# Kernel tuning notes

Hardware: AMD Instinct MI355X
Metric: run time of the kernel (lower is better)

Reference implementation:

```python
import jax, jax.numpy as jnp
import numpy as np

VOCAB = 256
HDC_DIM = 4096
DECAY = 0.95
B, T = 8, 2048


def setup_inputs() -> dict:
    key = jax.random.key(0)
    k_cb, k_idx = jax.random.split(key)
    # bipolar codebook: sign of gaussian, zeros mapped to +1 (prob-0 event but faithful)
    cb = jnp.sign(jax.random.normal(k_cb, (VOCAB, HDC_DIM), dtype=jnp.float32))
    cb = jnp.where(cb == 0, 1.0, cb)
    idx = jax.random.randint(k_idx, (B, T), 0, VOCAB)
    return {"char_codebook": cb, "idx": idx}


def _encode_trigrams(char_codebook, idx):
    chars = char_codebook[idx]                       # (B, T, D)
    chars_m1 = jnp.roll(chars, 1, axis=1).at[:, 0, :].set(0.0)
    chars_m2 = jnp.roll(chars, 2, axis=1).at[:, :2, :].set(0.0)
    trigrams = chars * jnp.roll(chars_m1, 1, axis=-1) * jnp.roll(chars_m2, 2, axis=-1)
    return 0.7 * trigrams + 0.3 * chars


def _decay_matrix(T, dtype):
    i = jnp.arange(T)
    diffs = (i[:, None] - i[None, :]).astype(dtype)  # (T, T)
    m = jnp.where(diffs >= 0, jnp.asarray(DECAY, dtype) ** diffs, 0.0)
    return m / jnp.sum(m, axis=-1, keepdims=True)    # row-normalized causal decay


def reference(char_codebook, idx):
    hdc = _encode_trigrams(char_codebook, idx)       # (B, T, D)
    M = _decay_matrix(hdc.shape[1], hdc.dtype)       # (T, T)
    # context[t] = sum_i M[t, i] * hdc[i]  -> one dense matmul as in the original
    return jnp.einsum("ts,bsd->btd", M, hdc)
```

## Files before the change

### kernel.cpp

```cpp
#include <hip/hip_runtime.h>


#define VOCAB   256
#define D_      4096
#define T_      2048
#define B_      8
#define DEC     0.95f
#define CHUNK   32
#define NCH     (T_/CHUNK)
#define THREADS 128
#define DGRP    (D_/(THREADS*8))
#define ROWB    (D_/8)

__device__ unsigned char g_P1[VOCAB*ROWB];
__device__ unsigned char g_P2[VOCAB*ROWB];
__device__ unsigned char g_P3[VOCAB*ROWB];
__device__ float g_invn[T_];
__device__ float g_S[B_*NCH*D_];
__device__ float g_C[B_*NCH*D_];

__global__ __launch_bounds__(256) void pack_kernel(const float* __restrict__ cb) {
    int gid = blockIdx.x * 256 + threadIdx.x;
    int r   = gid >> 9;
    int byt = gid & 511;
    const float* row = cb + r * D_;
    unsigned b1 = 0, b2 = 0, b3 = 0;
#pragma unroll
    for (int j = 0; j < 8; ++j) {
        int d = byt * 8 + j;
        unsigned s1 = __float_as_uint(row[d]) >> 31;
        unsigned s2 = __float_as_uint(row[(d - 1) & (D_ - 1)]) >> 31;
        unsigned s3 = __float_as_uint(row[(d - 2) & (D_ - 1)]) >> 31;
        b1 |= s1 << j; b2 |= s2 << j; b3 |= s3 << j;
    }
    g_P1[gid] = (unsigned char)b1;
    g_P2[gid] = (unsigned char)b2;
    g_P3[gid] = (unsigned char)b3;
    if (gid < T_)
        g_invn[gid] = (1.0f - DEC) / (1.0f - powf(DEC, (float)(gid + 1)));
}

__device__ __forceinline__ void bind_step(unsigned ub1, unsigned n8,
                                          float magp, float magn, float* acc) {
#pragma unroll
    for (int j = 0; j < 8; ++j) {
        float mag    = ((n8 >> j) & 1u) ? magn : magp;
        unsigned sgn = (ub1 << (31 - j)) & 0x80000000u;
        float v      = __uint_as_float(__float_as_uint(mag) ^ sgn);
        acc[j] = fmaf(acc[j], DEC, v);
    }
}

__global__ __launch_bounds__(THREADS) void states_kernel(const int* __restrict__ idx) {
    const int b  = blockIdx.z;
    const int ch = blockIdx.y;
    const int dg = blockIdx.x;
    const int t0 = ch * CHUNK;
    const int lo = (t0 - 2 > 0) ? (t0 - 2) : 0;

    __shared__ int sidx[CHUNK + 2];
    if (threadIdx.x < (unsigned)(t0 + CHUNK - lo))
        sidx[threadIdx.x] = idx[b * T_ + lo + threadIdx.x];
    __syncthreads();

    const int i = dg * THREADS + threadIdx.x;
    float acc[8];
#pragma unroll
    for (int j = 0; j < 8; ++j) acc[j] = 0.0f;

#pragma unroll 4
    for (int k = 0; k < CHUNK; ++k) {
        int t = t0 + k;
        int r1 = sidx[t - lo];
        unsigned ub1 = g_P1[r1 * ROWB + i];
        unsigned n8 = 0; float magp = 1.0f, magn = -0.4f;
        if (t >= 2) {
            int r2 = sidx[t - 1 - lo], r3 = sidx[t - 2 - lo];
            n8 = (unsigned)(g_P2[r2 * ROWB + i] ^ g_P3[r3 * ROWB + i]);
        } else { magp = 0.3f; magn = 0.3f; }
        bind_step(ub1, n8, magp, magn, acc);
    }

    float* S = g_S + (size_t)(b * NCH + ch) * D_ + (size_t)i * 8;
    ((float4*)S)[0] = make_float4(acc[0], acc[1], acc[2], acc[3]);
    ((float4*)S)[1] = make_float4(acc[4], acc[5], acc[6], acc[7]);
}

__global__ __launch_bounds__(256) void carry_kernel() {
    int g = blockIdx.x * 256 + threadIdx.x;
    int b = g >> 12;
    int d = g & (D_ - 1);
    float dch = powf(DEC, (float)CHUNK);
    float c = 0.0f;
#pragma unroll 8
    for (int ch = 0; ch < NCH; ++ch) {
        size_t o = (size_t)(b * NCH + ch) * D_ + d;
        g_C[o] = c;
        c = fmaf(c, dch, g_S[o]);
    }
}

__global__ __launch_bounds__(THREADS) void emit_kernel(const int* __restrict__ idx,
                                                       float* __restrict__ out) {
    const int b  = blockIdx.z;
    const int ch = blockIdx.y;
    const int dg = blockIdx.x;
    const int t0 = ch * CHUNK;
    const int lo = (t0 - 2 > 0) ? (t0 - 2) : 0;

    __shared__ int   sidx[CHUNK + 2];
    __shared__ float sinv[CHUNK];
    if (threadIdx.x < (unsigned)(t0 + CHUNK - lo))
        sidx[threadIdx.x] = idx[b * T_ + lo + threadIdx.x];
    if (threadIdx.x < CHUNK)
        sinv[threadIdx.x] = g_invn[t0 + threadIdx.x];
    __syncthreads();

    const int i = dg * THREADS + threadIdx.x;

    const float* C = g_C + (size_t)(b * NCH + ch) * D_ + (size_t)i * 8;
    float4 c0 = ((const float4*)C)[0];
    float4 c1 = ((const float4*)C)[1];
    float acc[8] = {c0.x, c0.y, c0.z, c0.w, c1.x, c1.y, c1.z, c1.w};

    float* ob = out + (size_t)(b * T_) * D_ + (size_t)i * 8;
#pragma unroll 4
    for (int k = 0; k < CHUNK; ++k) {
        int t = t0 + k;
        int r1 = sidx[t - lo];
        unsigned ub1 = g_P1[r1 * ROWB + i];
        unsigned n8 = 0; float magp = 1.0f, magn = -0.4f;
        if (t >= 2) {
            int r2 = sidx[t - 1 - lo], r3 = sidx[t - 2 - lo];
            n8 = (unsigned)(g_P2[r2 * ROWB + i] ^ g_P3[r3 * ROWB + i]);
        } else { magp = 0.3f; magn = 0.3f; }
        bind_step(ub1, n8, magp, magn, acc);

        float invn = sinv[k];
        float4* o = (float4*)(ob + (size_t)t * D_);
        o[0] = make_float4(acc[0]*invn, acc[1]*invn, acc[2]*invn, acc[3]*invn);
        o[1] = make_float4(acc[4]*invn, acc[5]*invn, acc[6]*invn, acc[7]*invn);
    }
}

extern "C" void kernel_launch(void* const* d_in, const int* in_sizes, int n_in,
                              void* d_out, int out_size, void* d_ws, size_t ws_size,
                              hipStream_t stream) {
    const float* cb  = (const float*)d_in[0];
    const int*   idx = (const int*)d_in[1];
    float*       out = (float*)d_out;

    pack_kernel  <<<dim3((VOCAB * ROWB) / 256), dim3(256), 0, stream>>>(cb);
    states_kernel<<<dim3(DGRP, NCH, B_), dim3(THREADS), 0, stream>>>(idx);
    carry_kernel <<<dim3((B_ * D_) / 256), dim3(256), 0, stream>>>();
    emit_kernel  <<<dim3(DGRP, NCH, B_), dim3(THREADS), 0, stream>>>(idx, out);
}
```

Before: 304.1 us.

## Replace chunked scan with warm-up recurrence fused into single emit kernel

```diff
diff --git a/kernel.cpp b/kernel.cpp
--- a/kernel.cpp
+++ b/kernel.cpp
@@ -6,18 +6,20 @@
 #define T_      2048
 #define B_      8
 #define DEC     0.95f
-#define CHUNK   32
-#define NCH     (T_/CHUNK)
+#define SEG     64
+#define NSEG    (T_/SEG)
+#define WARM    256
 #define THREADS 128
 #define DGRP    (D_/(THREADS*8))
 #define ROWB    (D_/8)
+#define SIDXN   (WARM + SEG + 2)
+
+typedef float f32x4 __attribute__((ext_vector_type(4)));
 
 __device__ unsigned char g_P1[VOCAB*ROWB];
 __device__ unsigned char g_P2[VOCAB*ROWB];
 __device__ unsigned char g_P3[VOCAB*ROWB];
 __device__ float g_invn[T_];
-__device__ float g_S[B_*NCH*D_];
-__device__ float g_C[B_*NCH*D_];
 
 __global__ __launch_bounds__(256) void pack_kernel(const float* __restrict__ cb) {
     int gid = blockIdx.x * 256 + threadIdx.x;
@@ -51,95 +53,63 @@
     }
 }
 
-__global__ __launch_bounds__(THREADS) void states_kernel(const int* __restrict__ idx) {
+__global__ __launch_bounds__(THREADS) void fused_kernel(const int* __restrict__ idx,
+                                                        float* __restrict__ out) {
     const int b  = blockIdx.z;
-    const int ch = blockIdx.y;
+    const int s  = blockIdx.y;
     const int dg = blockIdx.x;
-    const int t0 = ch * CHUNK;
-    const int lo = (t0 - 2 > 0) ? (t0 - 2) : 0;
+    const int t0 = s * SEG;
+    const int t1 = t0 + SEG;
+    const int tw = (t0 - WARM > 0) ? (t0 - WARM) : 0;
+    const int lo = (tw - 2 > 0) ? (tw - 2) : 0;
+    const int n  = t1 - lo;
 
-    __shared__ int sidx[CHUNK + 2];
-    if (threadIdx.x < (unsigned)(t0 + CHUNK - lo))
-        sidx[threadIdx.x] = idx[b * T_ + lo + threadIdx.x];
+    __shared__ int   sidx[SIDXN];
+    __shared__ float sinv[SEG];
+    for (int k = threadIdx.x; k < n; k += THREADS)
+        sidx[k] = idx[b * T_ + lo + k];
+    if (threadIdx.x < SEG)
+        sinv[threadIdx.x] = g_invn[t0 + threadIdx.x];
     __syncthreads();
 
     const int i = dg * THREADS + threadIdx.x;
+    const unsigned char* __restrict__ P1 = g_P1 + i;
+    const unsigned char* __restrict__ P2 = g_P2 + i;
+    const unsigned char* __restrict__ P3 = g_P3 + i;
+
     float acc[8];
 #pragma unroll
     for (int j = 0; j < 8; ++j) acc[j] = 0.0f;
 
 #pragma unroll 4
-    for (int k = 0; k < CHUNK; ++k) {
-        int t = t0 + k;
+    for (int t = tw; t < t0; ++t) {
         int r1 = sidx[t - lo];
-        unsigned ub1 = g_P1[r1 * ROWB + i];
+        unsigned ub1 = P1[r1 * ROWB];
         unsigned n8 = 0; float magp = 1.0f, magn = -0.4f;
         if (t >= 2) {
             int r2 = sidx[t - 1 - lo], r3 = sidx[t - 2 - lo];
-            n8 = (unsigned)(g_P2[r2 * ROWB + i] ^ g_P3[r3 * ROWB + i]);
+            n8 = (unsigned)(P2[r2 * ROWB] ^ P3[r3 * ROWB]);
         } else { magp = 0.3f; magn = 0.3f; }
         bind_step(ub1, n8, magp, magn, acc);
     }
 
-    float* S = g_S + (size_t)(b * NCH + ch) * D_ + (size_t)i * 8;
-    ((float4*)S)[0] = make_float4(acc[0], acc[1], acc[2], acc[3]);
-    ((float4*)S)[1] = make_float4(acc[4], acc[5], acc[6], acc[7]);
-}
-
-__global__ __launch_bounds__(256) void carry_kernel() {
-    int g = blockIdx.x * 256 + threadIdx.x;
-    int b = g >> 12;
-    int d = g & (D_ - 1);
-    float dch = powf(DEC, (float)CHUNK);
-    float c = 0.0f;
-#pragma unroll 8
-    for (int ch = 0; ch < NCH; ++ch) {
-        size_t o = (size_t)(b * NCH + ch) * D_ + d;
-        g_C[o] = c;
-        c = fmaf(c, dch, g_S[o]);
-    }
-}
-
-__global__ __launch_bounds__(THREADS) void emit_kernel(const int* __restrict__ idx,
-                                                       float* __restrict__ out) {
-    const int b  = blockIdx.z;
-    const int ch = blockIdx.y;
-    const int dg = blockIdx.x;
-    const int t0 = ch * CHUNK;
-    const int lo = (t0 - 2 > 0) ? (t0 - 2) : 0;
-
-    __shared__ int   sidx[CHUNK + 2];
-    __shared__ float sinv[CHUNK];
-    if (threadIdx.x < (unsigned)(t0 + CHUNK - lo))
-        sidx[threadIdx.x] = idx[b * T_ + lo + threadIdx.x];
-    if (threadIdx.x < CHUNK)
-        sinv[threadIdx.x] = g_invn[t0 + threadIdx.x];
-    __syncthreads();
-
-    const int i = dg * THREADS + threadIdx.x;
-
-    const float* C = g_C + (size_t)(b * NCH + ch) * D_ + (size_t)i * 8;
-    float4 c0 = ((const float4*)C)[0];
-    float4 c1 = ((const float4*)C)[1];
-    float acc[8] = {c0.x, c0.y, c0.z, c0.w, c1.x, c1.y, c1.z, c1.w};
-
     float* ob = out + (size_t)(b * T_) * D_ + (size_t)i * 8;
 #pragma unroll 4
-    for (int k = 0; k < CHUNK; ++k) {
+    for (int k = 0; k < SEG; ++k) {
         int t = t0 + k;
         int r1 = sidx[t - lo];
-        unsigned ub1 = g_P1[r1 * ROWB + i];
+        unsigned ub1 = P1[r1 * ROWB];
         unsigned n8 = 0; float magp = 1.0f, magn = -0.4f;
         if (t >= 2) {
             int r2 = sidx[t - 1 - lo], r3 = sidx[t - 2 - lo];
-            n8 = (unsigned)(g_P2[r2 * ROWB + i] ^ g_P3[r3 * ROWB + i]);
+            n8 = (unsigned)(P2[r2 * ROWB] ^ P3[r3 * ROWB]);
         } else { magp = 0.3f; magn = 0.3f; }
         bind_step(ub1, n8, magp, magn, acc);
 
         float invn = sinv[k];
-        float4* o = (float4*)(ob + (size_t)t * D_);
-        o[0] = make_float4(acc[0]*invn, acc[1]*invn, acc[2]*invn, acc[3]*invn);
-        o[1] = make_float4(acc[4]*invn, acc[5]*invn, acc[6]*invn, acc[7]*invn);
+        f32x4* o = (f32x4*)(ob + (size_t)t * D_);
+        o[0] = (f32x4){acc[0]*invn, acc[1]*invn, acc[2]*invn, acc[3]*invn};
+        o[1] = (f32x4){acc[4]*invn, acc[5]*invn, acc[6]*invn, acc[7]*invn};
     }
 }
 
@@ -150,8 +120,6 @@
     const int*   idx = (const int*)d_in[1];
     float*       out = (float*)d_out;
 
-    pack_kernel  <<<dim3((VOCAB * ROWB) / 256), dim3(256), 0, stream>>>(cb);
-    states_kernel<<<dim3(DGRP, NCH, B_), dim3(THREADS), 0, stream>>>(idx);
-    carry_kernel <<<dim3((B_ * D_) / 256), dim3(256), 0, stream>>>();
-    emit_kernel  <<<dim3(DGRP, NCH, B_), dim3(THREADS), 0, stream>>>(idx, out);
+    pack_kernel <<<dim3((VOCAB * ROWB) / 256), dim3(256), 0, stream>>>(cb);
+    fused_kernel<<<dim3(DGRP, NSEG, B_), dim3(THREADS), 0, stream>>>(idx, out);
 }
```

Measured after the change: 332.2 us. 9.2% more time.
